# Kernel optimization log

Measured on AMD Instinct MI355X. Metric: run time of the kernel, lower is better.

Reference implementation:

```python
import jax, jax.numpy as jnp
import numpy as np

B, N = 1, 512
C_S, C_Z, C_H, H, PQ, PV = 384, 128, 16, 12, 4, 8
INF, EPS = 1e5, 1e-8
HW_INIT = 0.541324854612918  # softplus^{-1}(1), ipa_point_weights_init_


def _rotary(t, rot_dim, theta=10000.0):
    # lucidrains interleaved rotary over residue axis (axis 1); rotates first rot_dim channels
    n = t.shape[1]
    inv_freq = 1.0 / (theta ** (jnp.arange(0, rot_dim, 2, dtype=jnp.float32) / rot_dim))
    freqs = jnp.arange(n, dtype=jnp.float32)[:, None] * inv_freq  # [N, rot_dim//2]
    cos = jnp.cos(freqs)[None, :, None, :].astype(t.dtype)
    sin = jnp.sin(freqs)[None, :, None, :].astype(t.dtype)
    tr, tp = t[..., :rot_dim], t[..., rot_dim:]
    x1, x2 = tr[..., 0::2], tr[..., 1::2]
    tr = jnp.stack([x1 * cos - x2 * sin, x1 * sin + x2 * cos], axis=-1).reshape(tr.shape)
    return jnp.concatenate([tr, tp], axis=-1)


def _ipa(s, z, rot, trans, mask, Wq, bq, Wkv, bkv, Wqp, bqp, Wkvp, bkvp, Wb, bb,
         head_weights, Whid, bhid, Wpair, bpair, Wpts, bpts, Wpn, bpn):
    Bx, Nx = s.shape[0], s.shape[1]
    q = (s @ Wq + bq).reshape(Bx, Nx, H, C_H)
    kv = (s @ Wkv + bkv).reshape(Bx, Nx, H, 2 * C_H)
    k, v = kv[..., :C_H], kv[..., C_H:]

    def make_pts(x, npts):
        # channel layout: [x-block, y-block, z-block] -> [B,N,H*npts,3], then rigid apply R@p+t
        x = jnp.stack(jnp.split(x, 3, axis=-1), axis=-1)
        x = jnp.einsum('bnij,bnpj->bnpi', rot, x) + trans[:, :, None, :]
        return x.reshape(Bx, Nx, H, npts, 3)

    q_pts = make_pts(s @ Wqp + bqp, PQ)
    kv_pts = make_pts(s @ Wkvp + bkvp, PQ + PV)
    k_pts, v_pts = kv_pts[..., :PQ, :], kv_pts[..., PQ:, :]

    q = _rotary(q, C_H // 2)
    k = _rotary(k, C_H // 2)

    a = jnp.einsum('bihc,bjhc->bhij', q, k) * np.sqrt(1.0 / (3 * C_H))
    a = a + np.sqrt(1.0 / 3.0) * (jnp.einsum('bijc,ch->bhij', z, Wb) + bb[None, :, None, None])
    d2 = jnp.sum((q_pts[:, :, None] - k_pts[:, None]) ** 2, axis=-1)  # [B,Ni,Nj,H,PQ]
    hw = jax.nn.softplus(head_weights) * np.sqrt(1.0 / (3 * (PQ * 9.0 / 2)))
    a = a + jnp.transpose(-0.5 * jnp.sum(d2 * hw[None, None, None, :, None], axis=-1), (0, 3, 1, 2))
    sq_mask = INF * (mask[:, :, None] * mask[:, None, :] - 1.0)
    a = jax.nn.softmax(a + sq_mask[:, None], axis=-1)  # [B,H,N,N]

    o = jnp.einsum('bhij,bjhc->bihc', a, v).reshape(Bx, Nx, H * C_H)
    o_pt = jnp.einsum('bhij,bjhpx->bihpx', a, v_pts)  # [B,N,H,PV,3]
    o_pt = jnp.einsum('bnji,bnhpj->bnhpi', rot, o_pt - trans[:, :, None, None, :])  # invert_apply
    o_pt_norm = jnp.sqrt(jnp.sum(o_pt ** 2, axis=-1) + EPS).reshape(Bx, Nx, H * PV)
    o_pt = o_pt.reshape(Bx, Nx, H * PV, 3)
    pts_feat = jnp.concatenate([o_pt[..., 0], o_pt[..., 1], o_pt[..., 2]], axis=-1)
    o_pair = jnp.einsum('bhij,bijc->bihc', a, z).reshape(Bx, Nx, H * C_Z)

    s_out = ((o @ Whid + bhid) + (o_pair @ Wpair + bpair)
             + (pts_feat @ Wpts + bpts) + (o_pt_norm @ Wpn + bpn))
    return s_out, a


def setup_inputs() -> dict:
    key = jax.random.key(0)
    ks = jax.random.split(key, 16)
    f = lambda i, shape: jax.random.normal(ks[i], shape, dtype=jnp.float32)
    sc = 0.02
    rot, _ = jnp.linalg.qr(f(2, (B, N, 3, 3)))
    return {
        's': f(0, (B, N, C_S)),
        'z': f(1, (B, N, N, C_Z)),
        'rot': rot,
        'trans': f(3, (B, N, 3)),
        'mask': jnp.ones((B, N), jnp.float32),
        'Wq': f(4, (C_S, H * C_H)) * sc, 'bq': jnp.zeros((H * C_H,), jnp.float32),
        'Wkv': f(5, (C_S, 2 * H * C_H)) * sc, 'bkv': jnp.zeros((2 * H * C_H,), jnp.float32),
        'Wqp': f(6, (C_S, H * PQ * 3)) * sc, 'bqp': jnp.zeros((H * PQ * 3,), jnp.float32),
        'Wkvp': f(7, (C_S, H * (PQ + PV) * 3)) * sc, 'bkvp': jnp.zeros((H * (PQ + PV) * 3,), jnp.float32),
        'Wb': f(8, (C_Z, H)) * sc, 'bb': jnp.zeros((H,), jnp.float32),
        'head_weights': jnp.full((H,), HW_INIT, jnp.float32),
        'Whid': f(9, (H * C_H, C_S)) * sc, 'bhid': jnp.zeros((C_S,), jnp.float32),
        'Wpair': f(10, (H * C_Z, C_S)) * sc, 'bpair': jnp.zeros((C_S,), jnp.float32),
        'Wpts': f(11, (H * PV * 3, C_S)) * sc, 'bpts': jnp.zeros((C_S,), jnp.float32),
        'Wpn': f(12, (H * PV, C_S)) * sc, 'bpn': jnp.zeros((C_S,), jnp.float32),
    }


def reference(s, z, rot, trans, mask, Wq, bq, Wkv, bkv, Wqp, bqp, Wkvp, bkvp, Wb, bb,
              head_weights, Whid, bhid, Wpair, bpair, Wpts, bpts, Wpn, bpn):
    return _ipa(s, z, rot, trans, mask, Wq, bq, Wkv, bkv, Wqp, bqp, Wkvp, bkvp, Wb, bb,
                head_weights, Whid, bhid, Wpair, bpair, Wpts, bpts, Wpn, bpn)
```

## Files before the change

### kernel.cpp

```cpp
#include <hip/hip_runtime.h>
#include <hip/hip_bf16.h>
#include <cmath>

#define N 512
#define C_S 384
#define C_Z 128
#define C_H 16
#define H 12
#define PQ 4
#define PV 8

#define NJC 4
#define JCHUNK (N / NJC)
#define NPART 2016
#define NFEAT 2112
#define NRAW 1152
#define KSPLIT 11
#define KCHUNK 192

#define WS_Q    0
#define WS_K    (WS_Q + N*H*C_H)
#define WS_SM   WS_K
#define WS_V    (WS_K + N*H*C_H)
#define WS_QP   (WS_V + N*H*C_H)
#define WS_KP   (WS_QP + N*H*PQ*3)
#define WS_VP   (WS_KP + N*H*PQ*3)
#define WS_PART (WS_VP + N*H*PV*3)
#define WS_FEAT (WS_PART + N*NJC*NPART)
#define WS_RAW  WS_PART
#define WS_KT   (WS_PART + 1200000)
#define WS_KPT  (WS_KT + 98304)
#define WS_WBT  (WS_KPT + 73728)
#define WS_FOUT WS_PART

__global__ __launch_bounds__(256) void k_gemm_proj(
    const float* __restrict__ s,
    const float* __restrict__ Wq,  const float* __restrict__ bq,
    const float* __restrict__ Wkv, const float* __restrict__ bkv,
    const float* __restrict__ Wqp, const float* __restrict__ bqp,
    const float* __restrict__ Wkvp,const float* __restrict__ bkvp,
    float* __restrict__ raw_out)
{
    const int m0 = blockIdx.x * 64;
    const int c0 = blockIdx.y * 64;
    const int t  = threadIdx.x;
    const int tc = t & 15;
    const int tm = t >> 4;

    __shared__ float st[64 * 33];
    __shared__ float wt[32 * 64];

    float acc[4][4];
#pragma unroll
    for (int u = 0; u < 4; ++u) {
        int col = c0 + tc*4 + u;
        const float* b; int cb;
        if (col < 192)      { b = bq;   cb = 0; }
        else if (col < 576) { b = bkv;  cb = 192; }
        else if (col < 720) { b = bqp;  cb = 576; }
        else                { b = bkvp; cb = 720; }
        float bv = b[col - cb];
#pragma unroll
        for (int r = 0; r < 4; ++r) acc[r][u] = bv;
    }

    for (int k0 = 0; k0 < C_S; k0 += 32) {
        __syncthreads();
        for (int e = t; e < 512; e += 256) {
            int row = e >> 3, kq = e & 7;
            float4 v = *(const float4*)&s[(size_t)(m0 + row)*C_S + k0 + kq*4];
            st[row*33 + kq*4 + 0] = v.x;
            st[row*33 + kq*4 + 1] = v.y;
            st[row*33 + kq*4 + 2] = v.z;
            st[row*33 + kq*4 + 3] = v.w;
        }
        for (int e = t; e < 512; e += 256) {
            int kk = e >> 4, c4 = e & 15;
            int col = c0 + c4*4;
            const float* W; int ncol, cb;
            if (col < 192)      { W = Wq;   ncol = 192; cb = 0; }
            else if (col < 576) { W = Wkv;  ncol = 384; cb = 192; }
            else if (col < 720) { W = Wqp;  ncol = 144; cb = 576; }
            else                { W = Wkvp; ncol = 432; cb = 720; }
            float4 v = *(const float4*)&W[(size_t)(k0 + kk)*ncol + (col - cb)];
            *(float4*)&wt[kk*64 + c4*4] = v;
        }
        __syncthreads();

#pragma unroll 8
        for (int kk = 0; kk < 32; ++kk) {
            float4 w = *(const float4*)&wt[kk*64 + tc*4];
            float sv[4];
#pragma unroll
            for (int r = 0; r < 4; ++r) sv[r] = st[(tm*4 + r)*33 + kk];
#pragma unroll
            for (int r = 0; r < 4; ++r) {
                acc[r][0] += sv[r] * w.x;
                acc[r][1] += sv[r] * w.y;
                acc[r][2] += sv[r] * w.z;
                acc[r][3] += sv[r] * w.w;
            }
        }
    }

#pragma unroll
    for (int r = 0; r < 4; ++r) {
        float4 o = make_float4(acc[r][0], acc[r][1], acc[r][2], acc[r][3]);
        *(float4*)&raw_out[(size_t)(m0 + tm*4 + r)*NRAW + c0 + tc*4] = o;
    }
}

__global__ __launch_bounds__(256) void k_post(
    const float* __restrict__ raw_in, const float* __restrict__ rot,
    const float* __restrict__ trans, const float* __restrict__ Wb,
    float* __restrict__ ws)
{
    const int n = blockIdx.x;
    const int t = threadIdx.x;
    __shared__ float raw[NRAW];

    for (int idx = t; idx < NRAW; idx += 256) raw[idx] = raw_in[(size_t)n*NRAW + idx];
    __syncthreads();

    if (n == 0) {
        for (int idx = t; idx < H*C_Z; idx += 256) {
            int h = idx >> 7, c = idx & 127;
            ws[WS_WBT + h*128 + c] = Wb[c*H + h];
        }
    }

    float R[9], T[3];
#pragma unroll
    for (int u = 0; u < 9; ++u) R[u] = rot[n*9 + u];
#pragma unroll
    for (int u = 0; u < 3; ++u) T[u] = trans[n*3 + u];

    float* q    = ws + WS_Q;
    float* v    = ws + WS_V;
    float* qp   = ws + WS_QP;
    float* vp   = ws + WS_VP;
    float* kT4  = ws + WS_KT;
    float* kpT4 = ws + WS_KPT;

    for (int idx = t; idx < 1152; idx += 256) {
        if (idx < 192) {
            int h = idx >> 4, c = idx & 15;
            float val;
            if (c < 8) {
                int f = c >> 1;
                float fr = (f == 0) ? 1.0f : (f == 1) ? 0.1f : (f == 2) ? 0.01f : 0.001f;
                float ang = (float)n * fr;
                float x1 = raw[h*16 + 2*f];
                float x2 = raw[h*16 + 2*f + 1];
                float cs = cosf(ang), sn = sinf(ang);
                val = (c & 1) ? (x1*sn + x2*cs) : (x1*cs - x2*sn);
            } else {
                val = raw[h*16 + c];
            }
            q[n*192 + idx] = val;
        } else if (idx < 384) {
            int o = idx - 192, h = o >> 4, c = o & 15;
            float val;
            if (c < 8) {
                int f = c >> 1;
                float fr = (f == 0) ? 1.0f : (f == 1) ? 0.1f : (f == 2) ? 0.01f : 0.001f;
                float ang = (float)n * fr;
                float x1 = raw[192 + h*32 + 2*f];
                float x2 = raw[192 + h*32 + 2*f + 1];
                float cs = cosf(ang), sn = sinf(ang);
                val = (c & 1) ? (x1*sn + x2*cs) : (x1*cs - x2*sn);
            } else {
                val = raw[192 + h*32 + c];
            }
            kT4[((size_t)(o >> 2)*N + n)*4 + (o & 3)] = val;
        } else if (idx < 576) {
            int o = idx - 384, h = o >> 4, c = o & 15;
            v[n*192 + o] = raw[192 + h*32 + 16 + c];
        } else if (idx < 720) {
            int o = idx - 576;
            int hp = o / 3, ic = o - hp*3;
            float acc = T[ic];
#pragma unroll
            for (int j = 0; j < 3; ++j) acc += R[ic*3 + j] * raw[576 + j*48 + hp];
            qp[n*144 + o] = acc;
        } else {
            int o = idx - 720;
            int hp = o / 3, ic = o - hp*3;
            int h = hp / 12, p = hp - h*12;
            float acc = T[ic];
#pragma unroll
            for (int j = 0; j < 3; ++j) acc += R[ic*3 + j] * raw[720 + j*144 + hp];
            if (p < PQ) {
                int e = h*12 + p*3 + ic;
                kpT4[((size_t)(e >> 2)*N + n)*4 + (e & 3)] = acc;
            } else {
                vp[n*(H*PV*3) + (h*PV + (p - PQ))*3 + ic] = acc;
            }
        }
    }
}

__global__ __launch_bounds__(256) void k_logits(
    float* __restrict__ ws, const float* __restrict__ z,
    const float* __restrict__ bb,
    const float* __restrict__ hwts, const float* __restrict__ mask,
    float* __restrict__ a_out)
{
    const int i  = blockIdx.x;
    const int j0 = blockIdx.y * 64;
    const int t  = threadIdx.x;
    const int j  = t & 63;
    const int jg = j0 + j;
    const int h0 = __builtin_amdgcn_readfirstlane(3 * (t >> 6));

    __shared__ float zt[64*68];

    float4 ra0, ra1, ra2, ra3, rb0, rb1, rb2, rb3;
    {
        const float* zbase = z + (((size_t)i*N) + j0)*C_Z;
        int e0 = t,       r0_ = e0 >> 4, c0_ = e0 & 15;
        int e1 = t + 256, r1_ = e1 >> 4, c1_ = e1 & 15;
        int e2 = t + 512, r2_ = e2 >> 4, c2_ = e2 & 15;
        int e3 = t + 768, r3_ = e3 >> 4, c3_ = e3 & 15;
        ra0 = *(const float4*)&zbase[(size_t)r0_*C_Z + c0_*4];
        ra1 = *(const float4*)&zbase[(size_t)r1_*C_Z + c1_*4];
        ra2 = *(const float4*)&zbase[(size_t)r2_*C_Z + c2_*4];
        ra3 = *(const float4*)&zbase[(size_t)r3_*C_Z + c3_*4];
        rb0 = *(const float4*)&zbase[(size_t)r0_*C_Z + 64 + c0_*4];
        rb1 = *(const float4*)&zbase[(size_t)r1_*C_Z + 64 + c1_*4];
        rb2 = *(const float4*)&zbase[(size_t)r2_*C_Z + 64 + c2_*4];
        rb3 = *(const float4*)&zbase[(size_t)r3_*C_Z + 64 + c3_*4];
    }

    const float* q    = ws + WS_Q  + (size_t)i*192;
    const float* qp   = ws + WS_QP + (size_t)i*144;
    const float* kT4  = ws + WS_KT;
    const float* kpT4 = ws + WS_KPT;

    const float c1 = sqrtf(1.0f / 48.0f);
    const float c2 = sqrtf(1.0f / 3.0f);
    const float mterm = 100000.0f * (mask[i] * mask[jg] - 1.0f);

    float qkd[3];
#pragma unroll
    for (int u = 0; u < 3; ++u) {
        const int h = h0 + u;
        float qk = 0.0f;
#pragma unroll
        for (int cq = 0; cq < 4; ++cq) {
            float4 kv = *(const float4*)&kT4[((size_t)(h*4 + cq)*N + jg)*4];
            qk += q[h*16 + cq*4 + 0]*kv.x + q[h*16 + cq*4 + 1]*kv.y
                + q[h*16 + cq*4 + 2]*kv.z + q[h*16 + cq*4 + 3]*kv.w;
        }
        float d2s = 0.0f;
#pragma unroll
        for (int eq = 0; eq < 3; ++eq) {
            float4 pv = *(const float4*)&kpT4[((size_t)(h*3 + eq)*N + jg)*4];
            float d;
            d = qp[h*12 + eq*4 + 0] - pv.x; d2s += d*d;
            d = qp[h*12 + eq*4 + 1] - pv.y; d2s += d*d;
            d = qp[h*12 + eq*4 + 2] - pv.z; d2s += d*d;
            d = qp[h*12 + eq*4 + 3] - pv.w; d2s += d*d;
        }
        float hw = log1pf(expf(hwts[h])) * sqrtf(1.0f / 54.0f);
        qkd[u] = c1*qk - 0.5f*hw*d2s + mterm + c2*bb[h];
    }

    {
        int e0 = t,       r0_ = e0 >> 4, c0_ = e0 & 15;
        int e1 = t + 256, r1_ = e1 >> 4, c1_ = e1 & 15;
        int e2 = t + 512, r2_ = e2 >> 4, c2_ = e2 & 15;
        int e3 = t + 768, r3_ = e3 >> 4, c3_ = e3 & 15;
        *(float4*)&zt[r0_*68 + c0_*4] = ra0;
        *(float4*)&zt[r1_*68 + c1_*4] = ra1;
        *(float4*)&zt[r2_*68 + c2_*4] = ra2;
        *(float4*)&zt[r3_*68 + c3_*4] = ra3;
    }
    __syncthreads();

    const float* w0 = ws + WS_WBT + (size_t)h0*128;
    float acc[3] = {0.0f, 0.0f, 0.0f};
#pragma unroll
    for (int c4 = 0; c4 < 16; ++c4) {
        float4 zv = *(const float4*)&zt[j*68 + c4*4];
        float4 b0 = *(const float4*)&w0[c4*4];
        float4 b1 = *(const float4*)&w0[128 + c4*4];
        float4 b2 = *(const float4*)&w0[256 + c4*4];
        acc[0] += zv.x*b0.x + zv.y*b0.y + zv.z*b0.z + zv.w*b0.w;
        acc[1] += zv.x*b1.x + zv.y*b1.y + zv.z*b1.z + zv.w*b1.w;
        acc[2] += zv.x*b2.x + zv.y*b2.y + zv.z*b2.z + zv.w*b2.w;
    }
    __syncthreads();

    {
        int e0 = t,       r0_ = e0 >> 4, c0_ = e0 & 15;
        int e1 = t + 256, r1_ = e1 >> 4, c1_ = e1 & 15;
        int e2 = t + 512, r2_ = e2 >> 4, c2_ = e2 & 15;
        int e3 = t + 768, r3_ = e3 >> 4, c3_ = e3 & 15;
        *(float4*)&zt[r0_*68 + c0_*4] = rb0;
        *(float4*)&zt[r1_*68 + c1_*4] = rb1;
        *(float4*)&zt[r2_*68 + c2_*4] = rb2;
        *(float4*)&zt[r3_*68 + c3_*4] = rb3;
    }
    __syncthreads();

#pragma unroll
    for (int c4 = 0; c4 < 16; ++c4) {
        float4 zv = *(const float4*)&zt[j*68 + c4*4];
        float4 b0 = *(const float4*)&w0[64 + c4*4];
        float4 b1 = *(const float4*)&w0[192 + c4*4];
        float4 b2 = *(const float4*)&w0[320 + c4*4];
        acc[0] += zv.x*b0.x + zv.y*b0.y + zv.z*b0.z + zv.w*b0.w;
        acc[1] += zv.x*b1.x + zv.y*b1.y + zv.z*b1.z + zv.w*b1.w;
        acc[2] += zv.x*b2.x + zv.y*b2.y + zv.z*b2.z + zv.w*b2.w;
    }

    float lgv[3];
#pragma unroll
    for (int u = 0; u < 3; ++u) {
        lgv[u] = qkd[u] + c2*acc[u];
        a_out[((size_t)(h0 + u)*N + i)*N + jg] = lgv[u];
    }

    float* sm = ws + WS_SM;
#pragma unroll
    for (int u = 0; u < 3; ++u) {
        float m = lgv[u];
#pragma unroll
        for (int off = 32; off; off >>= 1) m = fmaxf(m, __shfl_xor(m, off));
        float sme = expf(lgv[u] - m);
#pragma unroll
        for (int off = 32; off; off >>= 1) sme += __shfl_xor(sme, off);
        if (j == 0) {
            sm[(size_t)i*192 + (h0 + u)*16 + blockIdx.y*2 + 0] = m;
            sm[(size_t)i*192 + (h0 + u)*16 + blockIdx.y*2 + 1] = sme;
        }
    }
}

__global__ __launch_bounds__(256) void k_av(
    float* __restrict__ a_full, const float* __restrict__ ws_ro,
    const float* __restrict__ z, float* __restrict__ ws)
{
    const int i  = blockIdx.x;
    const int jc = blockIdx.y;
    const int j0 = jc * JCHUNK;
    const int t  = threadIdx.x;

    __shared__ float a_s[H*JCHUNK];
    __shared__ float Msm[12], Ism[12];

    const float* v  = ws_ro + WS_V;
    const float* vp = ws_ro + WS_VP;
    const float* sm = ws_ro + WS_SM;
    float* part = ws + WS_PART + ((size_t)i*NJC + jc)*NPART;

    if (t < 12) {
        const float* st = sm + (size_t)i*192 + t*16;
        float M = -1e30f;
#pragma unroll
        for (int q8 = 0; q8 < 8; ++q8) M = fmaxf(M, st[q8*2]);
        float S = 0.0f;
#pragma unroll
        for (int q8 = 0; q8 < 8; ++q8) S += st[q8*2 + 1] * expf(st[q8*2] - M);
        Msm[t] = M;
        Ism[t] = 1.0f / S;
    }
    __syncthreads();

    for (int e = t; e < H*JCHUNK; e += 256) {
        int h = e >> 7, jj = e & (JCHUNK-1);
        size_t gi = ((size_t)h*N + i)*N + j0 + jj;
        float val = expf(a_full[gi] - Msm[h]) * Ism[h];
        a_s[e] = val;
        a_full[gi] = val;
    }
    __syncthreads();

    for (int idx = t; idx < 480; idx += 256) {
        float acc = 0.0f;
        if (idx < 192) {
            int h = idx >> 4;
            const float* vv = v + (size_t)j0*192 + idx;
            const float* ar = &a_s[h*JCHUNK];
#pragma unroll 8
            for (int jj = 0; jj < JCHUNK; ++jj) acc += ar[jj] * vv[(size_t)jj*192];
        } else {
            int o = idx - 192;
            int h = (o/3) >> 3;
            const float* vv = vp + (size_t)j0*288 + o;
            const float* ar = &a_s[h*JCHUNK];
#pragma unroll 8
            for (int jj = 0; jj < JCHUNK; ++jj) acc += ar[jj] * vv[(size_t)jj*288];
        }
        part[idx] = acc;
    }

    {
        const int c  = t & 127;
        const int hb = t >> 7;
        float acc[6];
#pragma unroll
        for (int u = 0; u < 6; ++u) acc[u] = 0.0f;
        const float* zi = z + ((size_t)i*N + j0)*C_Z + c;
        for (int jj = 0; jj < JCHUNK; jj += 8) {
            float zr[8];
#pragma unroll
            for (int r = 0; r < 8; ++r) zr[r] = zi[(size_t)(jj+r)*C_Z];
            float4 av0[6], av1[6];
#pragma unroll
            for (int u = 0; u < 6; ++u) {
                av0[u] = *(const float4*)&a_s[(hb + 2*u)*JCHUNK + jj];
                av1[u] = *(const float4*)&a_s[(hb + 2*u)*JCHUNK + jj + 4];
            }
#pragma unroll
            for (int u = 0; u < 6; ++u) {
                acc[u] += av0[u].x*zr[0] + av0[u].y*zr[1] + av0[u].z*zr[2] + av0[u].w*zr[3];
                acc[u] += av1[u].x*zr[4] + av1[u].y*zr[5] + av1[u].z*zr[6] + av1[u].w*zr[7];
            }
        }
#pragma unroll
        for (int u = 0; u < 6; ++u) part[480 + (hb + 2*u)*C_Z + c] = acc[u];
    }
}

__global__ __launch_bounds__(256) void k_feat(
    const float* __restrict__ rot, const float* __restrict__ trans,
    float* __restrict__ ws)
{
    const int i = blockIdx.x;
    const int t = threadIdx.x;

    __shared__ float vec[NPART];

    const float* part = ws + WS_PART + (size_t)i*NJC*NPART;
    float* feat = ws + WS_FEAT + (size_t)i*NFEAT;

    for (int e = t; e < NPART; e += 256) {
        float acc = 0.0f;
#pragma unroll
        for (int jc = 0; jc < NJC; ++jc) acc += part[(size_t)jc*NPART + e];
        vec[e] = acc;
    }
    __syncthreads();

    for (int e = t; e < NPART; e += 256) {
        if (e < 192)       feat[e] = vec[e];
        else if (e >= 480) feat[192 + (e - 480)] = vec[e];
    }

    if (t < H*PV) {
        const int hp = t;
        float T0 = trans[i*3+0], T1 = trans[i*3+1], T2 = trans[i*3+2];
        float px = vec[192 + hp*3 + 0] - T0;
        float py = vec[192 + hp*3 + 1] - T1;
        float pz = vec[192 + hp*3 + 2] - T2;
        const float* R = rot + i*9;
        float ox = R[0]*px + R[3]*py + R[6]*pz;
        float oy = R[1]*px + R[4]*py + R[7]*pz;
        float oz = R[2]*px + R[5]*py + R[8]*pz;
        feat[1728 + hp]       = ox;
        feat[1728 + 96 + hp]  = oy;
        feat[1728 + 192 + hp] = oz;
        feat[2016 + hp] = sqrtf(ox*ox + oy*oy + oz*oz + 1e-8f);
    }
}

__global__ __launch_bounds__(256) void k_final_part(
    const float* __restrict__ ws,
    const float* __restrict__ Whid, const float* __restrict__ Wpair,
    const float* __restrict__ Wpts, const float* __restrict__ Wpn,
    float* __restrict__ fout)
{
    const int m0 = blockIdx.x * 64;
    const int c0 = blockIdx.y * 64;
    const int kc = blockIdx.z;
    const int t  = threadIdx.x;
    const int tc = t & 15;
    const int tm = t >> 4;

    __shared__ float ft[64 * 33];
    __shared__ float wt[32 * 64];

    const float* feat = ws + WS_FEAT;

    float acc[4][4];
#pragma unroll
    for (int r = 0; r < 4; ++r)
#pragma unroll
        for (int u = 0; u < 4; ++u) acc[r][u] = 0.0f;

    const int kbase = kc * KCHUNK;
    for (int k0 = kbase; k0 < kbase + KCHUNK; k0 += 32) {
        const float* W; int r0;
        if (k0 < 192)       { W = Whid;  r0 = k0; }
        else if (k0 < 1728) { W = Wpair; r0 = k0 - 192; }
        else if (k0 < 2016) { W = Wpts;  r0 = k0 - 1728; }
        else                { W = Wpn;   r0 = k0 - 2016; }

        __syncthreads();
        for (int e = t; e < 512; e += 256) {
            int row = e >> 3, kq = e & 7;
            float4 v = *(const float4*)&feat[(size_t)(m0 + row)*NFEAT + k0 + kq*4];
            ft[row*33 + kq*4 + 0] = v.x;
            ft[row*33 + kq*4 + 1] = v.y;
            ft[row*33 + kq*4 + 2] = v.z;
            ft[row*33 + kq*4 + 3] = v.w;
        }
        for (int e = t; e < 512; e += 256) {
            int kk = e >> 4, c4 = e & 15;
            float4 v = *(const float4*)&W[(size_t)(r0 + kk)*C_S + c0 + c4*4];
            *(float4*)&wt[kk*64 + c4*4] = v;
        }
        __syncthreads();

#pragma unroll 8
        for (int kk = 0; kk < 32; ++kk) {
            float4 w = *(const float4*)&wt[kk*64 + tc*4];
            float sv[4];
#pragma unroll
            for (int r = 0; r < 4; ++r) sv[r] = ft[(tm*4 + r)*33 + kk];
#pragma unroll
            for (int r = 0; r < 4; ++r) {
                acc[r][0] += sv[r] * w.x;
                acc[r][1] += sv[r] * w.y;
                acc[r][2] += sv[r] * w.z;
                acc[r][3] += sv[r] * w.w;
            }
        }
    }

#pragma unroll
    for (int r = 0; r < 4; ++r) {
        float4 o = make_float4(acc[r][0], acc[r][1], acc[r][2], acc[r][3]);
        *(float4*)&fout[((size_t)kc*N + m0 + tm*4 + r)*C_S + c0 + tc*4] = o;
    }
}

__global__ __launch_bounds__(256) void k_red(
    const float* __restrict__ fout,
    const float* __restrict__ bhid, const float* __restrict__ bpair,
    const float* __restrict__ bpts, const float* __restrict__ bpn,
    float* __restrict__ s_out)
{
    const int idx = blockIdx.x * 256 + threadIdx.x;
    const int c = idx % C_S;
    float acc = bhid[c] + bpair[c] + bpts[c] + bpn[c];
#pragma unroll
    for (int kc = 0; kc < KSPLIT; ++kc)
        acc += fout[(size_t)kc*N*C_S + idx];
    s_out[idx] = acc;
}

extern "C" void kernel_launch(void* const* d_in, const int* in_sizes, int n_in,
                              void* d_out, int out_size, void* d_ws, size_t ws_size,
                              hipStream_t stream) {
    const float* s     = (const float*)d_in[0];
    const float* z     = (const float*)d_in[1];
    const float* rot   = (const float*)d_in[2];
    const float* trans = (const float*)d_in[3];
    const float* mask  = (const float*)d_in[4];
    const float* Wq    = (const float*)d_in[5];
    const float* bq    = (const float*)d_in[6];
    const float* Wkv   = (const float*)d_in[7];
    const float* bkv   = (const float*)d_in[8];
    const float* Wqp   = (const float*)d_in[9];
    const float* bqp   = (const float*)d_in[10];
    const float* Wkvp  = (const float*)d_in[11];
    const float* bkvp  = (const float*)d_in[12];
    const float* Wb    = (const float*)d_in[13];
    const float* bb    = (const float*)d_in[14];
    const float* hwts  = (const float*)d_in[15];
    const float* Whid  = (const float*)d_in[16];
    const float* bhid  = (const float*)d_in[17];
    const float* Wpair = (const float*)d_in[18];
    const float* bpair = (const float*)d_in[19];
    const float* Wpts  = (const float*)d_in[20];
    const float* bpts  = (const float*)d_in[21];
    const float* Wpn   = (const float*)d_in[22];
    const float* bpn   = (const float*)d_in[23];

    float* out   = (float*)d_out;
    float* s_out = out;
    float* a_out = out + N*C_S;
    float* ws    = (float*)d_ws;

    k_gemm_proj<<<dim3(8, 18), 256, 0, stream>>>(s, Wq, bq, Wkv, bkv, Wqp, bqp,
                                                 Wkvp, bkvp, ws + WS_RAW);
    k_post<<<N, 256, 0, stream>>>(ws + WS_RAW, rot, trans, Wb, ws);
    k_logits<<<dim3(N, 8), 256, 0, stream>>>(ws, z, bb, hwts, mask, a_out);
    k_av<<<dim3(N, NJC), 256, 0, stream>>>(a_out, ws, z, ws);
    k_feat<<<N, 256, 0, stream>>>(rot, trans, ws);
    k_final_part<<<dim3(8, 6, KSPLIT), 256, 0, stream>>>(ws, Whid, Wpair, Wpts,
                                                         Wpn, ws + WS_FOUT);
    k_red<<<(N*C_S)/256, 256, 0, stream>>>(ws + WS_FOUT, bhid, bpair, bpts, bpn,
                                           s_out);
}
```

Baseline: 157.3 us.

## Split projection GEMM over K, vectorize z-contraction and partial reduction loads

The projection GEMM is split three ways along the reduction dimension, with each split writing its own slab, and k_post sums the slabs when it loads them. This raises the block count from 144 to 432 so more of the GPU is busy. The pair-feature contraction in k_av is remapped so each thread handles two channels with float2 z loads and three heads. The partial-sum reduction in k_feat now uses float4 loads. In exchange, the workspace offset for the transposed buffers moves to make room for the extra slabs, and k_post does more global reads.

```diff
diff --git a/kernel.cpp b/kernel.cpp
--- a/kernel.cpp
+++ b/kernel.cpp
@@ -17,6 +17,7 @@
 #define NRAW 1152
 #define KSPLIT 11
 #define KCHUNK 192
+#define PSPLIT 3
 
 #define WS_Q    0
 #define WS_K    (WS_Q + N*H*C_H)
@@ -28,7 +29,7 @@
 #define WS_PART (WS_VP + N*H*PV*3)
 #define WS_FEAT (WS_PART + N*NJC*NPART)
 #define WS_RAW  WS_PART
-#define WS_KT   (WS_PART + 1200000)
+#define WS_KT   (WS_PART + 2000000)
 #define WS_KPT  (WS_KT + 98304)
 #define WS_WBT  (WS_KPT + 73728)
 #define WS_FOUT WS_PART
@@ -43,6 +44,7 @@
 {
     const int m0 = blockIdx.x * 64;
     const int c0 = blockIdx.y * 64;
+    const int kc = blockIdx.z;
     const int t  = threadIdx.x;
     const int tc = t & 15;
     const int tm = t >> 4;
@@ -51,20 +53,28 @@
     __shared__ float wt[32 * 64];
 
     float acc[4][4];
-#pragma unroll
-    for (int u = 0; u < 4; ++u) {
-        int col = c0 + tc*4 + u;
-        const float* b; int cb;
-        if (col < 192)      { b = bq;   cb = 0; }
-        else if (col < 576) { b = bkv;  cb = 192; }
-        else if (col < 720) { b = bqp;  cb = 576; }
-        else                { b = bkvp; cb = 720; }
-        float bv = b[col - cb];
-#pragma unroll
-        for (int r = 0; r < 4; ++r) acc[r][u] = bv;
-    }
-
-    for (int k0 = 0; k0 < C_S; k0 += 32) {
+    if (kc == 0) {
+#pragma unroll
+        for (int u = 0; u < 4; ++u) {
+            int col = c0 + tc*4 + u;
+            const float* b; int cb;
+            if (col < 192)      { b = bq;   cb = 0; }
+            else if (col < 576) { b = bkv;  cb = 192; }
+            else if (col < 720) { b = bqp;  cb = 576; }
+            else                { b = bkvp; cb = 720; }
+            float bv = b[col - cb];
+#pragma unroll
+            for (int r = 0; r < 4; ++r) acc[r][u] = bv;
+        }
+    } else {
+#pragma unroll
+        for (int u = 0; u < 4; ++u)
+#pragma unroll
+            for (int r = 0; r < 4; ++r) acc[r][u] = 0.0f;
+    }
+
+    const int kbase = kc * 128;
+    for (int k0 = kbase; k0 < kbase + 128; k0 += 32) {
         __syncthreads();
         for (int e = t; e < 512; e += 256) {
             int row = e >> 3, kq = e & 7;
@@ -103,10 +113,11 @@
         }
     }
 
+    float* slab = raw_out + (size_t)kc*N*NRAW;
 #pragma unroll
     for (int r = 0; r < 4; ++r) {
         float4 o = make_float4(acc[r][0], acc[r][1], acc[r][2], acc[r][3]);
-        *(float4*)&raw_out[(size_t)(m0 + tm*4 + r)*NRAW + c0 + tc*4] = o;
+        *(float4*)&slab[(size_t)(m0 + tm*4 + r)*NRAW + c0 + tc*4] = o;
     }
 }
 
@@ -119,7 +130,12 @@
     const int t = threadIdx.x;
     __shared__ float raw[NRAW];
 
-    for (int idx = t; idx < NRAW; idx += 256) raw[idx] = raw_in[(size_t)n*NRAW + idx];
+    for (int idx = t; idx < NRAW; idx += 256) {
+        float a0 = raw_in[(size_t)n*NRAW + idx];
+        float a1 = raw_in[(size_t)N*NRAW + (size_t)n*NRAW + idx];
+        float a2 = raw_in[2*(size_t)N*NRAW + (size_t)n*NRAW + idx];
+        raw[idx] = a0 + a1 + a2;
+    }
     __syncthreads();
 
     if (n == 0) {
@@ -397,30 +413,31 @@
     }
 
     {
-        const int c  = t & 127;
-        const int hb = t >> 7;
-        float acc[6];
-#pragma unroll
-        for (int u = 0; u < 6; ++u) acc[u] = 0.0f;
-        const float* zi = z + ((size_t)i*N + j0)*C_Z + c;
-        for (int jj = 0; jj < JCHUNK; jj += 8) {
-            float zr[8];
-#pragma unroll
-            for (int r = 0; r < 8; ++r) zr[r] = zi[(size_t)(jj+r)*C_Z];
-            float4 av0[6], av1[6];
-#pragma unroll
-            for (int u = 0; u < 6; ++u) {
-                av0[u] = *(const float4*)&a_s[(hb + 2*u)*JCHUNK + jj];
-                av1[u] = *(const float4*)&a_s[(hb + 2*u)*JCHUNK + jj + 4];
+        const int c2 = t & 63;
+        const int hb = t >> 6;
+        float acc0[3] = {0,0,0}, acc1[3] = {0,0,0};
+        const float* zi = z + ((size_t)i*N + j0)*C_Z + 2*c2;
+#pragma unroll 4
+        for (int jj = 0; jj < JCHUNK; jj += 4) {
+            float2 z0 = *(const float2*)&zi[(size_t)(jj+0)*C_Z];
+            float2 z1 = *(const float2*)&zi[(size_t)(jj+1)*C_Z];
+            float2 z2 = *(const float2*)&zi[(size_t)(jj+2)*C_Z];
+            float2 z3 = *(const float2*)&zi[(size_t)(jj+3)*C_Z];
+            float4 av[3];
+#pragma unroll
+            for (int u = 0; u < 3; ++u)
+                av[u] = *(const float4*)&a_s[(hb*3 + u)*JCHUNK + jj];
+#pragma unroll
+            for (int u = 0; u < 3; ++u) {
+                acc0[u] += av[u].x*z0.x + av[u].y*z1.x + av[u].z*z2.x + av[u].w*z3.x;
+                acc1[u] += av[u].x*z0.y + av[u].y*z1.y + av[u].z*z2.y + av[u].w*z3.y;
             }
-#pragma unroll
-            for (int u = 0; u < 6; ++u) {
-                acc[u] += av0[u].x*zr[0] + av0[u].y*zr[1] + av0[u].z*zr[2] + av0[u].w*zr[3];
-                acc[u] += av1[u].x*zr[4] + av1[u].y*zr[5] + av1[u].z*zr[6] + av1[u].w*zr[7];
-            }
-        }
-#pragma unroll
-        for (int u = 0; u < 6; ++u) part[480 + (hb + 2*u)*C_Z + c] = acc[u];
+        }
+#pragma unroll
+        for (int u = 0; u < 3; ++u) {
+            part[480 + (hb*3 + u)*C_Z + 2*c2 + 0] = acc0[u];
+            part[480 + (hb*3 + u)*C_Z + 2*c2 + 1] = acc1[u];
+        }
     }
 }
 
@@ -436,11 +453,14 @@
     const float* part = ws + WS_PART + (size_t)i*NJC*NPART;
     float* feat = ws + WS_FEAT + (size_t)i*NFEAT;
 
-    for (int e = t; e < NPART; e += 256) {
-        float acc = 0.0f;
-#pragma unroll
-        for (int jc = 0; jc < NJC; ++jc) acc += part[(size_t)jc*NPART + e];
-        vec[e] = acc;
+    for (int e4 = t; e4 < 504; e4 += 256) {
+        float4 acc = make_float4(0.f, 0.f, 0.f, 0.f);
+#pragma unroll
+        for (int jc = 0; jc < NJC; ++jc) {
+            float4 p = *(const float4*)&part[(size_t)jc*NPART + e4*4];
+            acc.x += p.x; acc.y += p.y; acc.z += p.z; acc.w += p.w;
+        }
+        *(float4*)&vec[e4*4] = acc;
     }
     __syncthreads();
 
@@ -585,8 +605,9 @@
     float* a_out = out + N*C_S;
     float* ws    = (float*)d_ws;
 
-    k_gemm_proj<<<dim3(8, 18), 256, 0, stream>>>(s, Wq, bq, Wkv, bkv, Wqp, bqp,
-                                                 Wkvp, bkvp, ws + WS_RAW);
+    k_gemm_proj<<<dim3(8, 18, PSPLIT), 256, 0, stream>>>(s, Wq, bq, Wkv, bkv,
+                                                         Wqp, bqp, Wkvp, bkvp,
+                                                         ws + WS_RAW);
     k_post<<<N, 256, 0, stream>>>(ws + WS_RAW, rot, trans, Wb, ws);
     k_logits<<<dim3(N, 8), 256, 0, stream>>>(ws, z, bb, hwts, mask, a_out);
     k_av<<<dim3(N, NJC), 256, 0, stream>>>(a_out, ws, z, ws);
```

Measured after the change: 149.8 us. 4.8% less time.
